# Performance work log

Measured on AMD Instinct MI355X. Metric: run time of the kernel, lower is better.

## Reference

```python
import jax, jax.numpy as jnp
import numpy as np
import math

COV_WEIGHT = 1.0
BANDWIDTH_FACTOR = 1.06
SQRT_2PI = math.sqrt(2.0 * math.pi)
EPS_LOG = 1e-8
H_MIN = 1e-4


def setup_inputs() -> dict:
    key = jax.random.key(0)
    activity = jax.random.normal(key, (2048, 64), dtype=jnp.float32)
    return {"activity": activity}


def reference(activity):
    B, R = activity.shape
    # Silverman bandwidth per receptor (torch .std uses ddof=1)
    std = jnp.std(activity, axis=0, ddof=1)                     # (R,)
    h = jnp.maximum(BANDWIDTH_FACTOR * std * (B ** (-0.2)), H_MIN)  # (R,)

    # Pairwise Gaussian KDE: query == samples == activity
    u = (activity[:, None, :] - activity[None, :, :]) / h       # (B_q, B_s, R)
    kernel_values = jnp.exp(-0.5 * u * u) / SQRT_2PI             # (B_q, B_s, R)
    density = kernel_values.sum(axis=1) / (B * h)                # (B_q, R)

    entropies = -jnp.mean(jnp.log(density + EPS_LOG), axis=0)    # (R,)
    loss_entropy = -entropies.mean()

    # Covariance penalty: sum of squared off-diagonals
    centered = activity - activity.mean(axis=0, keepdims=True)
    cov = (centered.T @ centered) / (B - 1)                      # (R, R)
    off = cov - jnp.diag(jnp.diag(cov))
    loss_cov = jnp.sum(off * off)

    total_loss = loss_entropy + COV_WEIGHT * loss_cov
    return total_loss
```

## Files before the change

kernel.cpp:

```cpp
#include <hip/hip_runtime.h>
#include <math.h>

#define B_SZ 2048
#define R_SZ 64
#define QT 8
#define NSPLIT 2
#define KDE_BLOCKS (B_SZ / QT * NSPLIT)

#define B_POW_NEG02 0.217637640824031f
#define SQRT_2PI 2.5066282746310002f
#define LOG2E 1.44269504088896340736f

extern "C" __device__ float __ocml_native_exp2_f32(float);

typedef __attribute__((ext_vector_type(2))) float f32x2;


__global__ __launch_bounds__(1024) void cov_stats_kernel(const float* __restrict__ A,
                                                         float* __restrict__ U,
                                                         float* __restrict__ density,
                                                         float* __restrict__ lscale,
                                                         float* __restrict__ cov_partial,
                                                         float* __restrict__ ent_acc,
                                                         int* __restrict__ done2) {
    int i = blockIdx.x;
    int tid = threadIdx.x;
    int j = tid & 63, bg = tid >> 6;

    float g = 0.f, sj = 0.f, s2j = 0.f;
#pragma unroll 4
    for (int b = bg; b < B_SZ; b += 16) {
        float ai = A[b * R_SZ + i];
        float aj = A[b * R_SZ + j];
        g = fmaf(ai, aj, g);
        sj += aj;
        s2j = fmaf(aj, aj, s2j);
    }

    __shared__ float gred[16][64], sred[16][64], s2red[16][64];
    __shared__ float gfin[64], sfin[64], hs[64];
    gred[bg][j] = g; sred[bg][j] = sj; s2red[bg][j] = s2j;
    __syncthreads();
    if (tid < 64) {
        float G = 0.f, S = 0.f, S2 = 0.f;
#pragma unroll
        for (int t = 0; t < 16; ++t) { G += gred[t][j]; S += sred[t][j]; S2 += s2red[t][j]; }
        gfin[j] = G;
        sfin[j] = S;
        float m = S * (1.f / (float)B_SZ);
        float var = (S2 - S * m) * (1.f / (float)(B_SZ - 1));
        var = fmaxf(var, 0.f);
        float h = fmaxf(1.06f * sqrtf(var) * B_POW_NEG02, 1e-4f);
        hs[j] = sqrtf(0.5f * LOG2E) / h;
        if (i == 0) lscale[j] = 1.0f / ((float)B_SZ * h * SQRT_2PI);
    }
    __syncthreads();
    if (tid < 64) {
        float m_j = sfin[j] * (1.f / (float)B_SZ);
        float m_i = sfin[i] * (1.f / (float)B_SZ);
        float cov = (gfin[j] - (float)B_SZ * m_i * m_j) * (1.f / (float)(B_SZ - 1));
        float v = (j == i) ? 0.f : cov * cov;
        for (int off = 32; off > 0; off >>= 1) v += __shfl_down(v, off, 64);
        if (j == 0) cov_partial[i] = v;
    }
    if (i == 0 && tid == 64) { *ent_acc = 0.f; *done2 = 0; }

    int base = i * (32 * R_SZ);
    float k0 = hs[tid & 63];
    U[base + tid]        = A[base + tid]        * k0;
    U[base + 1024 + tid] = A[base + 1024 + tid] * k0;
    density[base + tid] = 0.f;
    density[base + 1024 + tid] = 0.f;
}

__global__ __launch_bounds__(1024) void kde_kernel(const float* __restrict__ U,
                                                   float* __restrict__ density) {
    int tid = threadIdx.x;
    int r = tid & 63, sg = tid >> 6;
    int g = blockIdx.x >> 1;
    int half = blockIdx.x & 1;
    int q0 = g * QT;

    f32x2 uq01 = { U[(q0 + 0) * R_SZ + r], U[(q0 + 1) * R_SZ + r] };
    f32x2 uq23 = { U[(q0 + 2) * R_SZ + r], U[(q0 + 3) * R_SZ + r] };
    f32x2 uq45 = { U[(q0 + 4) * R_SZ + r], U[(q0 + 5) * R_SZ + r] };
    f32x2 uq67 = { U[(q0 + 6) * R_SZ + r], U[(q0 + 7) * R_SZ + r] };
    f32x2 c01 = { 0.f, 0.f }, c23 = { 0.f, 0.f };
    f32x2 c45 = { 0.f, 0.f }, c67 = { 0.f, 0.f };

#define KDE_BODY(usv)                                                          \
    {                                                                          \
        f32x2 uss = { (usv), (usv) };                                          \
        f32x2 d01 = uq01 - uss, d23 = uq23 - uss;                              \
        f32x2 d45 = uq45 - uss, d67 = uq67 - uss;                              \
        f32x2 n01 = -d01 * d01, n23 = -d23 * d23;                              \
        f32x2 n45 = -d45 * d45, n67 = -d67 * d67;                              \
        f32x2 e01 = { __ocml_native_exp2_f32(n01.x), __ocml_native_exp2_f32(n01.y) }; \
        f32x2 e23 = { __ocml_native_exp2_f32(n23.x), __ocml_native_exp2_f32(n23.y) }; \
        f32x2 e45 = { __ocml_native_exp2_f32(n45.x), __ocml_native_exp2_f32(n45.y) }; \
        f32x2 e67 = { __ocml_native_exp2_f32(n67.x), __ocml_native_exp2_f32(n67.y) }; \
        c01 += e01; c23 += e23; c45 += e45; c67 += e67;                        \
    }

    const float* Up = U + (half * 1024 + sg) * R_SZ + r;
    float p[8];
#pragma unroll
    for (int j = 0; j < 8; ++j) p[j] = Up[j * 1024];

    int li = 8 * 1024;
#pragma unroll 1
    for (int k = 0; k < 7; ++k) {
#pragma unroll
        for (int j = 0; j < 8; ++j) {
            float us = p[j];
            p[j] = Up[li + j * 1024];
            KDE_BODY(us);
        }
        li += 8 * 1024;
    }
#pragma unroll
    for (int j = 0; j < 8; ++j) KDE_BODY(p[j]);

#undef KDE_BODY

    __shared__ float red[16][QT][64];
    red[sg][0][r] = c01.x; red[sg][1][r] = c01.y;
    red[sg][2][r] = c23.x; red[sg][3][r] = c23.y;
    red[sg][4][r] = c45.x; red[sg][5][r] = c45.y;
    red[sg][6][r] = c67.x; red[sg][7][r] = c67.y;
    __syncthreads();
    if (sg < QT) {
        float S = 0.f;
#pragma unroll
        for (int t = 0; t < 16; ++t) S += red[t][sg][r];
        unsafeAtomicAdd(&density[(q0 + sg) * R_SZ + r], S);
    }
}

__global__ __launch_bounds__(1024) void entropy_kernel(const float* __restrict__ density,
                                                       const float* __restrict__ lscale,
                                                       const float* __restrict__ cov_partial,
                                                       float* __restrict__ ent_acc,
                                                       int* __restrict__ done2,
                                                       float* __restrict__ out) {
    int tid = threadIdx.x;
    int r = tid & 63, sg = tid >> 6;
    float ls = lscale[r];
    int f = blockIdx.x * 2048 + tid;
    float v = __logf(fmaf(density[f], ls, 1e-8f))
            + __logf(fmaf(density[f + 1024], ls, 1e-8f));
    for (int off = 32; off > 0; off >>= 1) v += __shfl_down(v, off, 64);
    __shared__ float wr[16];
    if (r == 0) wr[sg] = v;
    __syncthreads();
    __shared__ int lastflag;
    if (tid == 0) {
        float s = 0.f;
#pragma unroll
        for (int w = 0; w < 16; ++w) s += wr[w];
        atomicAdd(ent_acc, s);
        __threadfence();
        int prev = atomicAdd(done2, 1);
        lastflag = (prev == 63);
    }
    __syncthreads();
    if (lastflag && tid < 64) {
        __threadfence();
        float v2 = cov_partial[tid];
        for (int off = 32; off > 0; off >>= 1) v2 += __shfl_down(v2, off, 64);
        if (tid == 0) {
            float ent = __hip_atomic_load(ent_acc, __ATOMIC_ACQUIRE,
                                          __HIP_MEMORY_SCOPE_AGENT);
            out[0] = ent * (1.0f / ((float)B_SZ * (float)R_SZ)) + v2;
        }
    }
}

extern "C" void kernel_launch(void* const* d_in, const int* in_sizes, int n_in,
                              void* d_out, int out_size, void* d_ws, size_t ws_size,
                              hipStream_t stream) {
    const float* A = (const float*)d_in[0];
    float* out = (float*)d_out;

    float* wsf = (float*)d_ws;
    float* lscale      = wsf;
    float* cov_partial = wsf + 64;
    float* ent_acc     = wsf + 160;
    int*   done2       = (int*)(wsf + 192);
    float* U           = wsf + 256;
    float* density     = wsf + 256 + B_SZ * R_SZ;

    cov_stats_kernel<<<R_SZ, 1024, 0, stream>>>(A, U, density, lscale, cov_partial,
                                                ent_acc, done2);
    kde_kernel<<<KDE_BLOCKS, 1024, 0, stream>>>(U, density);
    entropy_kernel<<<64, 1024, 0, stream>>>(density, lscale, cov_partial,
                                            ent_acc, done2, out);
}
```

Before: 100.3 us.

## Fuse bandwidth stats into KDE kernel and move covariance to epilogue

The separate stats kernel and the precomputed scaled copy U are removed. Each KDE block now recomputes the column mean and variance of A itself and scales the query and sample values on the fly. The split of samples across two blocks is dropped, so each block covers all 2048 samples and writes density directly with no atomics or zero-init. The covariance Gram computation moves into the epilogue kernel, which also recomputes the log scale. This cuts one launch and one global round trip, at the cost of redundant per-block column reductions, an extra multiply in the inner loop, and half as many KDE blocks.

```diff
diff --git a/kernel.cpp b/kernel.cpp
--- a/kernel.cpp
+++ b/kernel.cpp
@@ -4,8 +4,7 @@
 #define B_SZ 2048
 #define R_SZ 64
 #define QT 8
-#define NSPLIT 2
-#define KDE_BLOCKS (B_SZ / QT * NSPLIT)
+#define KDE_BLOCKS (B_SZ / QT)
 
 #define B_POW_NEG02 0.217637640824031f
 #define SQRT_2PI 2.5066282746310002f
@@ -16,75 +15,46 @@
 typedef __attribute__((ext_vector_type(2))) float f32x2;
 
 
-__global__ __launch_bounds__(1024) void cov_stats_kernel(const float* __restrict__ A,
-                                                         float* __restrict__ U,
+__global__ __launch_bounds__(1024) void kde_fused_kernel(const float* __restrict__ A,
                                                          float* __restrict__ density,
-                                                         float* __restrict__ lscale,
-                                                         float* __restrict__ cov_partial,
                                                          float* __restrict__ ent_acc,
                                                          int* __restrict__ done2) {
-    int i = blockIdx.x;
     int tid = threadIdx.x;
-    int j = tid & 63, bg = tid >> 6;
-
-    float g = 0.f, sj = 0.f, s2j = 0.f;
-#pragma unroll 4
-    for (int b = bg; b < B_SZ; b += 16) {
-        float ai = A[b * R_SZ + i];
-        float aj = A[b * R_SZ + j];
-        g = fmaf(ai, aj, g);
-        sj += aj;
-        s2j = fmaf(aj, aj, s2j);
-    }
-
-    __shared__ float gred[16][64], sred[16][64], s2red[16][64];
-    __shared__ float gfin[64], sfin[64], hs[64];
-    gred[bg][j] = g; sred[bg][j] = sj; s2red[bg][j] = s2j;
+    int r = tid & 63, sg = tid >> 6;
+
+    float s = 0.f, s2 = 0.f;
+    {
+        const float* Ac = A + sg * (128 * R_SZ) + r;
+#pragma unroll 8
+        for (int b = 0; b < 128; ++b) {
+            float v = Ac[b * R_SZ];
+            s += v;
+            s2 = fmaf(v, v, s2);
+        }
+    }
+    __shared__ float sred[16][64], s2red[16][64];
+    __shared__ float ksh[64];
+    sred[sg][r] = s; s2red[sg][r] = s2;
     __syncthreads();
     if (tid < 64) {
-        float G = 0.f, S = 0.f, S2 = 0.f;
-#pragma unroll
-        for (int t = 0; t < 16; ++t) { G += gred[t][j]; S += sred[t][j]; S2 += s2red[t][j]; }
-        gfin[j] = G;
-        sfin[j] = S;
+        float S = 0.f, S2 = 0.f;
+#pragma unroll
+        for (int t = 0; t < 16; ++t) { S += sred[t][tid]; S2 += s2red[t][tid]; }
         float m = S * (1.f / (float)B_SZ);
         float var = (S2 - S * m) * (1.f / (float)(B_SZ - 1));
         var = fmaxf(var, 0.f);
         float h = fmaxf(1.06f * sqrtf(var) * B_POW_NEG02, 1e-4f);
-        hs[j] = sqrtf(0.5f * LOG2E) / h;
-        if (i == 0) lscale[j] = 1.0f / ((float)B_SZ * h * SQRT_2PI);
-    }
-    __syncthreads();
-    if (tid < 64) {
-        float m_j = sfin[j] * (1.f / (float)B_SZ);
-        float m_i = sfin[i] * (1.f / (float)B_SZ);
-        float cov = (gfin[j] - (float)B_SZ * m_i * m_j) * (1.f / (float)(B_SZ - 1));
-        float v = (j == i) ? 0.f : cov * cov;
-        for (int off = 32; off > 0; off >>= 1) v += __shfl_down(v, off, 64);
-        if (j == 0) cov_partial[i] = v;
-    }
-    if (i == 0 && tid == 64) { *ent_acc = 0.f; *done2 = 0; }
-
-    int base = i * (32 * R_SZ);
-    float k0 = hs[tid & 63];
-    U[base + tid]        = A[base + tid]        * k0;
-    U[base + 1024 + tid] = A[base + 1024 + tid] * k0;
-    density[base + tid] = 0.f;
-    density[base + 1024 + tid] = 0.f;
-}
-
-__global__ __launch_bounds__(1024) void kde_kernel(const float* __restrict__ U,
-                                                   float* __restrict__ density) {
-    int tid = threadIdx.x;
-    int r = tid & 63, sg = tid >> 6;
-    int g = blockIdx.x >> 1;
-    int half = blockIdx.x & 1;
-    int q0 = g * QT;
-
-    f32x2 uq01 = { U[(q0 + 0) * R_SZ + r], U[(q0 + 1) * R_SZ + r] };
-    f32x2 uq23 = { U[(q0 + 2) * R_SZ + r], U[(q0 + 3) * R_SZ + r] };
-    f32x2 uq45 = { U[(q0 + 4) * R_SZ + r], U[(q0 + 5) * R_SZ + r] };
-    f32x2 uq67 = { U[(q0 + 6) * R_SZ + r], U[(q0 + 7) * R_SZ + r] };
+        ksh[tid] = sqrtf(0.5f * LOG2E) / h;
+    }
+    if (blockIdx.x == 0 && tid == 64) { *ent_acc = 0.f; *done2 = 0; }
+    __syncthreads();
+    float k = ksh[r];
+
+    int q0 = blockIdx.x * QT;
+    f32x2 uq01 = { A[(q0 + 0) * R_SZ + r] * k, A[(q0 + 1) * R_SZ + r] * k };
+    f32x2 uq23 = { A[(q0 + 2) * R_SZ + r] * k, A[(q0 + 3) * R_SZ + r] * k };
+    f32x2 uq45 = { A[(q0 + 4) * R_SZ + r] * k, A[(q0 + 5) * R_SZ + r] * k };
+    f32x2 uq67 = { A[(q0 + 6) * R_SZ + r] * k, A[(q0 + 7) * R_SZ + r] * k };
     f32x2 c01 = { 0.f, 0.f }, c23 = { 0.f, 0.f };
     f32x2 c45 = { 0.f, 0.f }, c67 = { 0.f, 0.f };
 
@@ -102,25 +72,27 @@
         c01 += e01; c23 += e23; c45 += e45; c67 += e67;                        \
     }
 
-    const float* Up = U + (half * 1024 + sg) * R_SZ + r;
+    const float* Up = A + sg * R_SZ + r;
     float p[8];
 #pragma unroll
-    for (int j = 0; j < 8; ++j) p[j] = Up[j * 1024];
+    for (int jj = 0; jj < 8; ++jj) p[jj] = Up[jj * 1024];
 
     int li = 8 * 1024;
 #pragma unroll 1
-    for (int k = 0; k < 7; ++k) {
-#pragma unroll
-        for (int j = 0; j < 8; ++j) {
-            float us = p[j];
-            p[j] = Up[li + j * 1024];
+    for (int kk = 0; kk < 15; ++kk) {
+#pragma unroll
+        for (int jj = 0; jj < 8; ++jj) {
+            float us = p[jj] * k;
+            p[jj] = Up[li + jj * 1024];
             KDE_BODY(us);
         }
         li += 8 * 1024;
     }
 #pragma unroll
-    for (int j = 0; j < 8; ++j) KDE_BODY(p[j]);
-
+    for (int jj = 0; jj < 8; ++jj) {
+        float us = p[jj] * k;
+        KDE_BODY(us);
+    }
 #undef KDE_BODY
 
     __shared__ float red[16][QT][64];
@@ -133,32 +105,70 @@
         float S = 0.f;
 #pragma unroll
         for (int t = 0; t < 16; ++t) S += red[t][sg][r];
-        unsafeAtomicAdd(&density[(q0 + sg) * R_SZ + r], S);
+        density[(q0 + sg) * R_SZ + r] = S;
     }
 }
 
-__global__ __launch_bounds__(1024) void entropy_kernel(const float* __restrict__ density,
-                                                       const float* __restrict__ lscale,
-                                                       const float* __restrict__ cov_partial,
-                                                       float* __restrict__ ent_acc,
-                                                       int* __restrict__ done2,
-                                                       float* __restrict__ out) {
+__global__ __launch_bounds__(1024) void epilogue_kernel(const float* __restrict__ A,
+                                                        const float* __restrict__ density,
+                                                        float* __restrict__ cov_partial,
+                                                        float* __restrict__ ent_acc,
+                                                        int* __restrict__ done2,
+                                                        float* __restrict__ out) {
+    int i = blockIdx.x;
     int tid = threadIdx.x;
-    int r = tid & 63, sg = tid >> 6;
-    float ls = lscale[r];
-    int f = blockIdx.x * 2048 + tid;
+    int j = tid & 63, bg = tid >> 6;
+
+    float g = 0.f, sj = 0.f, s2j = 0.f;
+#pragma unroll 4
+    for (int b = bg; b < B_SZ; b += 16) {
+        float ai = A[b * R_SZ + i];
+        float aj = A[b * R_SZ + j];
+        g = fmaf(ai, aj, g);
+        sj += aj;
+        s2j = fmaf(aj, aj, s2j);
+    }
+
+    __shared__ float gred[16][64], sred[16][64], s2red[16][64];
+    __shared__ float gfin[64], sfin[64], lsh[64];
+    gred[bg][j] = g; sred[bg][j] = sj; s2red[bg][j] = s2j;
+    __syncthreads();
+    if (tid < 64) {
+        float G = 0.f, S = 0.f, S2 = 0.f;
+#pragma unroll
+        for (int t = 0; t < 16; ++t) { G += gred[t][j]; S += sred[t][j]; S2 += s2red[t][j]; }
+        gfin[j] = G;
+        sfin[j] = S;
+        float m = S * (1.f / (float)B_SZ);
+        float var = (S2 - S * m) * (1.f / (float)(B_SZ - 1));
+        var = fmaxf(var, 0.f);
+        float h = fmaxf(1.06f * sqrtf(var) * B_POW_NEG02, 1e-4f);
+        lsh[j] = 1.0f / ((float)B_SZ * h * SQRT_2PI);
+    }
+    __syncthreads();
+    if (tid < 64) {
+        float m_j = sfin[j] * (1.f / (float)B_SZ);
+        float m_i = sfin[i] * (1.f / (float)B_SZ);
+        float cov = (gfin[j] - (float)B_SZ * m_i * m_j) * (1.f / (float)(B_SZ - 1));
+        float v = (j == i) ? 0.f : cov * cov;
+        for (int off = 32; off > 0; off >>= 1) v += __shfl_down(v, off, 64);
+        if (j == 0) cov_partial[i] = v;
+    }
+
+    float ls = lsh[j];
+    int f = i * 2048 + tid;
     float v = __logf(fmaf(density[f], ls, 1e-8f))
             + __logf(fmaf(density[f + 1024], ls, 1e-8f));
     for (int off = 32; off > 0; off >>= 1) v += __shfl_down(v, off, 64);
     __shared__ float wr[16];
-    if (r == 0) wr[sg] = v;
+    if (j == 0) wr[bg] = v;
     __syncthreads();
     __shared__ int lastflag;
     if (tid == 0) {
-        float s = 0.f;
-#pragma unroll
-        for (int w = 0; w < 16; ++w) s += wr[w];
-        atomicAdd(ent_acc, s);
+        float sE = 0.f;
+#pragma unroll
+        for (int w = 0; w < 16; ++w) sE += wr[w];
+        atomicAdd(ent_acc, sE);
         __threadfence();
         int prev = atomicAdd(done2, 1);
         lastflag = (prev == 63);
@@ -183,16 +193,12 @@
     float* out = (float*)d_out;
 
     float* wsf = (float*)d_ws;
-    float* lscale      = wsf;
-    float* cov_partial = wsf + 64;
-    float* ent_acc     = wsf + 160;
-    int*   done2       = (int*)(wsf + 192);
-    float* U           = wsf + 256;
-    float* density     = wsf + 256 + B_SZ * R_SZ;
-
-    cov_stats_kernel<<<R_SZ, 1024, 0, stream>>>(A, U, density, lscale, cov_partial,
-                                                ent_acc, done2);
-    kde_kernel<<<KDE_BLOCKS, 1024, 0, stream>>>(U, density);
-    entropy_kernel<<<64, 1024, 0, stream>>>(density, lscale, cov_partial,
-                                            ent_acc, done2, out);
+    float* cov_partial = wsf;
+    float* ent_acc     = wsf + 96;
+    int*   done2       = (int*)(wsf + 128);
+    float* density     = wsf + 256;
+
+    kde_fused_kernel<<<KDE_BLOCKS, 1024, 0, stream>>>(A, density, ent_acc, done2);
+    epilogue_kernel<<<R_SZ, 1024, 0, stream>>>(A, density, cov_partial,
+                                               ent_acc, done2, out);
 }
```

After: 100.2 us. About the same (-0.1%).
